# Kernel optimization log

Hardware: AMD Instinct MI355X
Metric: run time of the kernel (lower is better)

## Reference

```python
import jax, jax.numpy as jnp
import numpy as np

D_MODEL = 1024
N_HEAD = 16
HEAD_DIM = D_MODEL // N_HEAD


def setup_inputs() -> dict:
    key = jax.random.key(0)
    k1, k2, k3 = jax.random.split(key, 3)
    B, T = 2, 2048
    x = jax.random.normal(k1, (B, T, D_MODEL), dtype=jnp.float32)
    # nn.MultiheadAttention packed in-projection: (3*D, D), xavier-like scale
    w_in = jax.random.normal(k2, (3 * D_MODEL, D_MODEL), dtype=jnp.float32) * (1.0 / np.sqrt(D_MODEL))
    b_in = jnp.zeros((3 * D_MODEL,), dtype=jnp.float32)
    w_out = jax.random.normal(k3, (D_MODEL, D_MODEL), dtype=jnp.float32) * (1.0 / np.sqrt(D_MODEL))
    b_out = jnp.zeros((D_MODEL,), dtype=jnp.float32)
    return {"x": x, "w_in": w_in, "b_in": b_in, "w_out": w_out, "b_out": b_out}


def reference(x, w_in, b_in, w_out, b_out):
    B, T, D = x.shape
    H, hd = N_HEAD, HEAD_DIM
    # packed QKV projection (torch Linear convention: y = x @ W.T + b)
    qkv = x @ w_in.T + b_in                      # [B, T, 3D]
    q, k, v = jnp.split(qkv, 3, axis=-1)
    # [B, H, T, hd]
    q = q.reshape(B, T, H, hd).transpose(0, 2, 1, 3)
    k = k.reshape(B, T, H, hd).transpose(0, 2, 1, 3)
    v = v.reshape(B, T, H, hd).transpose(0, 2, 1, 3)
    scale = 1.0 / np.sqrt(hd).astype(np.float32)
    scores = jnp.einsum("bhqd,bhkd->bhqk", q * scale, k)  # [B, H, T, T]
    causal = jnp.tril(jnp.ones((T, T), dtype=bool))
    scores = jnp.where(causal, scores, jnp.finfo(scores.dtype).min)
    attn = jax.nn.softmax(scores, axis=-1)
    ctx = jnp.einsum("bhqk,bhkd->bhqd", attn, v)           # [B, H, T, hd]
    ctx = ctx.transpose(0, 2, 1, 3).reshape(B, T, D)
    return ctx @ w_out.T + b_out
```

## Files before the change

kernel.cpp:

```cpp
#include <hip/hip_runtime.h>


#define T_SEQ 2048
#define D_MODEL 1024
#define NEG_BIG (-1.0e30f)
#define Q_SCALE 0.18033688f

typedef float f32x4 __attribute__((ext_vector_type(4)));
typedef short s16x8 __attribute__((ext_vector_type(8)));
typedef __bf16 bf16x8 __attribute__((ext_vector_type(8)));

__device__ __forceinline__ f32x4 mfma16(s16x8 a, s16x8 b, f32x4 c) {
    return __builtin_amdgcn_mfma_f32_16x16x32_bf16(
        __builtin_bit_cast(bf16x8, a), __builtin_bit_cast(bf16x8, b), c, 0, 0, 0);
}

__device__ __forceinline__ short f2bf(float f) {
    unsigned int u = __float_as_uint(f);
    u += 0x7fffu + ((u >> 16) & 1u);
    return (short)(u >> 16);
}
__device__ __forceinline__ unsigned f2bfu(float f) {
    unsigned int u = __float_as_uint(f);
    u += 0x7fffu + ((u >> 16) & 1u);
    return u >> 16;
}
__device__ __forceinline__ unsigned f2bfu_fast(float f) {
    return (__float_as_uint(f) + 0x8000u) >> 16;
}
__device__ __forceinline__ float bf2f(short s) {
    return __uint_as_float(((unsigned int)(unsigned short)s) << 16);
}

__device__ __forceinline__ void async_lds16(const short* g, short* l) {
    __builtin_amdgcn_global_load_lds(
        (const __attribute__((address_space(1))) unsigned int*)g,
        (__attribute__((address_space(3))) unsigned int*)l, 16, 0, 0);
}

#define N_X   4194304
#define N_WI  3145728
#define N_BI  3072
#define N_WO  1048576
#define N_BO  1024
#define V_X   (N_X  / 4)
#define V_WI  (N_WI / 4)
#define V_BI  (N_BI / 4)
#define V_WO  (N_WO / 4)
#define V_BO  (N_BO / 4)
#define V_TOT (V_X + V_WI + V_BI + V_WO + V_BO)

__global__ __launch_bounds__(256) void canon_all_kernel(
    const float* __restrict__ x, const float* __restrict__ wi,
    const float* __restrict__ bi, const float* __restrict__ wo,
    const float* __restrict__ bo,
    short* __restrict__ xb, short* __restrict__ wib, short* __restrict__ bib,
    short* __restrict__ wob, short* __restrict__ bob)
{
    int i = blockIdx.x * 256 + threadIdx.x;
    if (i >= V_TOT) return;
    const float* src; short* dst; int off;
    if      (i < V_X)                    { src = x;  dst = xb;  off = i; }
    else if (i < V_X+V_WI)               { src = wi; dst = wib; off = i - V_X; }
    else if (i < V_X+V_WI+V_BI)          { src = bi; dst = bib; off = i - V_X - V_WI; }
    else if (i < V_X+V_WI+V_BI+V_WO)     { src = wo; dst = wob; off = i - V_X - V_WI - V_BI; }
    else                                 { src = bo; dst = bob; off = i - V_X - V_WI - V_BI - V_WO; }
    float4 v = ((const float4*)src)[off];
    short4 o = { f2bf(v.x), f2bf(v.y), f2bf(v.z), f2bf(v.w) };
    ((short4*)dst)[off] = o;
}

__global__ __launch_bounds__(256) void gemm_qkv_kernel(
    const short* __restrict__ A, const short* __restrict__ B,
    const short* __restrict__ bias,
    short* __restrict__ qo, short* __restrict__ ko, short* __restrict__ vo)
{
    const int K = 1024;
    alignas(16) __shared__ short As[128][32];
    alignas(16) __shared__ short Bs[128][32];
    const int m0 = blockIdx.x * 128;
    const int n0 = blockIdx.y * 128;
    const int tid = threadIdx.x;
    const int lane = tid & 63;
    const int w = tid >> 6;
    const int wm = (w >> 1) * 64, wn = (w & 1) * 64;
    const int quad = lane >> 4, l16 = lane & 15;

    f32x4 acc[4][4];
    const f32x4 zero = {0.f, 0.f, 0.f, 0.f};
#pragma unroll
    for (int i = 0; i < 4; ++i)
#pragma unroll
        for (int j = 0; j < 4; ++j) acc[i][j] = zero;

    const int lrow = lane >> 2;
    const int lcol = (lane & 3) * 8;
    const short* gA0 = &A[(m0 + w*32      + lrow) * K + lcol];
    const short* gA1 = &A[(m0 + w*32 + 16 + lrow) * K + lcol];
    const short* gB0 = &B[(n0 + w*32      + lrow) * K + lcol];
    const short* gB1 = &B[(n0 + w*32 + 16 + lrow) * K + lcol];
    short* lA0 = &As[w*32][0];
    short* lA1 = &As[w*32 + 16][0];
    short* lB0 = &Bs[w*32][0];
    short* lB1 = &Bs[w*32 + 16][0];

    for (int k0 = 0; k0 < K; k0 += 32) {
        __syncthreads();
        async_lds16(gA0 + k0, lA0);
        async_lds16(gA1 + k0, lA1);
        async_lds16(gB0 + k0, lB0);
        async_lds16(gB1 + k0, lB1);
        __syncthreads();

        s16x8 af[4], bfr[4];
#pragma unroll
        for (int i = 0; i < 4; ++i) af[i]  = *(const s16x8*)&As[wm + i*16 + l16][quad*8];
#pragma unroll
        for (int j = 0; j < 4; ++j) bfr[j] = *(const s16x8*)&Bs[wn + j*16 + l16][quad*8];
#pragma unroll
        for (int i = 0; i < 4; ++i)
#pragma unroll
            for (int j = 0; j < 4; ++j)
                acc[i][j] = mfma16(af[i], bfr[j], acc[i][j]);
    }

#pragma unroll
    for (int j = 0; j < 4; ++j) {
        int n = n0 + wn + j*16 + l16;
        float bi = bf2f(bias[n]);
        int which = n >> 10;
        short* dst = (which == 0) ? qo : (which == 1) ? ko : vo;
        float scl = (which == 0) ? Q_SCALE : 1.0f;
        int h = (n >> 6) & 15, d = n & 63;
#pragma unroll
        for (int i = 0; i < 4; ++i) {
#pragma unroll
            for (int r = 0; r < 4; ++r) {
                int m = m0 + wm + i*16 + quad*4 + r;
                int b = m >> 11, t = m & 2047;
                float v = (acc[i][j][r] + bi) * scl;
                dst[(((b*16 + h) * 2048) + t) * 64 + d] = f2bf(v);
            }
        }
    }
}

__global__ __launch_bounds__(256) void transpose_v_kernel(
    const short* __restrict__ V, short* __restrict__ Vt)
{
    alignas(16) __shared__ short buf[64][72];
    const int bh = blockIdx.x;
    const int t0 = blockIdx.y * 64;
    const int tid = threadIdx.x;
    const int r = tid >> 2;
    const int c = (tid & 3) * 16;

    const short* src = V + ((size_t)bh * T_SEQ + t0) * 64;
    *(float4*)&buf[r][c]     = *(const float4*)&src[r * 64 + c];
    *(float4*)&buf[r][c + 8] = *(const float4*)&src[r * 64 + c + 8];
    __syncthreads();

    s16x8 o0, o1;
#pragma unroll
    for (int k2 = 0; k2 < 8; ++k2) {
        o0[k2] = buf[c + k2][r];
        o1[k2] = buf[c + 8 + k2][r];
    }
    short* dst = Vt + ((size_t)bh * 64 + r) * T_SEQ + t0;
    *(s16x8*)&dst[c]     = o0;
    *(s16x8*)&dst[c + 8] = o1;
}

__global__ __launch_bounds__(256) void attn_kernel(
    const short* __restrict__ Q, const short* __restrict__ K,
    const short* __restrict__ Vt, short* __restrict__ ctx)
{
    alignas(16) __shared__ short Ks[64][72];
    alignas(16) __shared__ short Vs[64][72];
    alignas(16) __shared__ short Pl[4][32][72];

    const int bh = blockIdx.x;
    const int qt = 15 - (int)blockIdx.y;
    const int qbase = qt * 128;
    const int tid = threadIdx.x;
    const int w = tid >> 6, lane = tid & 63;
    const int quad = lane >> 4, l16 = lane & 15;
    const int b = bh >> 4, h = bh & 15;

    const short* Qb  = Q  + bh * T_SEQ * 64;
    const short* Kb  = K  + bh * T_SEQ * 64;
    const short* Vbt = Vt + (size_t)bh * 64 * T_SEQ;

    s16x8 qa0[2], qa1[2];
#pragma unroll
    for (int qs = 0; qs < 2; ++qs) {
        const short* qrow = Qb + (qbase + qs*64 + w*16 + l16) * 64;
        qa0[qs] = *(const s16x8*)(qrow + quad*8);
        qa1[qs] = *(const s16x8*)(qrow + 32 + quad*8);
    }

    const f32x4 zero = {0.f, 0.f, 0.f, 0.f};
    f32x4 o[2][4];
#pragma unroll
    for (int qs = 0; qs < 2; ++qs)
#pragma unroll
        for (int dt = 0; dt < 4; ++dt) o[qs][dt] = zero;
    float lsum[2] = {0.f, 0.f};

    const int sr = tid >> 2;
    const int sc = (tid & 3) * 16;

    for (int s0 = 0; s0 <= qbase + 64; s0 += 64) {
        __syncthreads();
        *(float4*)&Ks[sr][sc]     = *(const float4*)&Kb[(s0 + sr) * 64 + sc];
        *(float4*)&Ks[sr][sc + 8] = *(const float4*)&Kb[(s0 + sr) * 64 + sc + 8];
        *(float4*)&Vs[sr][sc]     = *(const float4*)&Vbt[(size_t)sr * T_SEQ + s0 + sc];
        *(float4*)&Vs[sr][sc + 8] = *(const float4*)&Vbt[(size_t)sr * T_SEQ + s0 + sc + 8];
        __syncthreads();

        const bool f0 = (s0 <= qbase);

        s16x8 ka0[4], ka1[4];
#pragma unroll
        for (int sub = 0; sub < 4; ++sub) {
            ka0[sub] = *(const s16x8*)&Ks[sub*16 + l16][quad*8];
            ka1[sub] = *(const s16x8*)&Ks[sub*16 + l16][32 + quad*8];
        }

#pragma unroll
        for (int qs = 0; qs < 2; ++qs) {
            if (qs == 0 && !f0) continue;
            const int fqb = qbase + qs*64;
            const int qg = fqb + w*16 + l16;
#pragma unroll
            for (int sub = 0; sub < 4; ++sub) {
                f32x4 S = mfma16(ka1[sub], qa1[qs], mfma16(ka0[sub], qa0[qs], zero));
                if (s0 == fqb) {
                    int sb = s0 + sub*16 + quad*4;
#pragma unroll
                    for (int r = 0; r < 4; ++r)
                        if (sb + r > qg) S[r] = NEG_BIG;
                }
                float p0 = exp2f(S[0]), p1 = exp2f(S[1]);
                float p2 = exp2f(S[2]), p3 = exp2f(S[3]);
                lsum[qs] += (p0 + p1) + (p2 + p3);
                uint2 pk;
                pk.x = f2bfu_fast(p0) | (f2bfu_fast(p1) << 16);
                pk.y = f2bfu_fast(p2) | (f2bfu_fast(p3) << 16);
                *(uint2*)&Pl[w][qs*16 + l16][sub*16 + quad*4] = pk;
            }
        }

        s16x8 va0[4], va1[4];
#pragma unroll
        for (int dt = 0; dt < 4; ++dt) {
            va0[dt] = *(const s16x8*)&Vs[dt*16 + l16][quad*8];
            va1[dt] = *(const s16x8*)&Vs[dt*16 + l16][32 + quad*8];
        }

#pragma unroll
        for (int qs = 0; qs < 2; ++qs) {
            if (qs == 0 && !f0) continue;
            s16x8 pb0 = *(const s16x8*)&Pl[w][qs*16 + l16][quad*8];
            s16x8 pb1 = *(const s16x8*)&Pl[w][qs*16 + l16][32 + quad*8];
#pragma unroll
            for (int dt = 0; dt < 4; ++dt)
                o[qs][dt] = mfma16(va1[dt], pb1, mfma16(va0[dt], pb0, o[qs][dt]));
        }
    }

#pragma unroll
    for (int qs = 0; qs < 2; ++qs) {
        float l = lsum[qs];
        l += __shfl_xor(l, 16, 64);
        l += __shfl_xor(l, 32, 64);
        float inv = 1.0f / l;
        int qg = qbase + qs*64 + w*16 + l16;
        int base = (b * T_SEQ + qg) * D_MODEL + h * 64;
#pragma unroll
        for (int dt = 0; dt < 4; ++dt) {
            uint2 pk;
            pk.x = f2bfu(o[qs][dt][0] * inv) | (f2bfu(o[qs][dt][1] * inv) << 16);
            pk.y = f2bfu(o[qs][dt][2] * inv) | (f2bfu(o[qs][dt][3] * inv) << 16);
            *(uint2*)&ctx[base + dt*16 + quad*4] = pk;
        }
    }
}

__global__ __launch_bounds__(256) void gemm_out_kernel(
    const short* __restrict__ A, const short* __restrict__ B,
    const short* __restrict__ bias, float* __restrict__ out)
{
    const int K = 1024;
    alignas(16) __shared__ short As[128][32];
    alignas(16) __shared__ short Bs[64][32];
    const int m0 = blockIdx.x * 128;
    const int n0 = blockIdx.y * 64;
    const int tid = threadIdx.x;
    const int lane = tid & 63;
    const int w = tid >> 6;
    const int wm = (w >> 1) * 64, wn = (w & 1) * 32;
    const int quad = lane >> 4, l16 = lane & 15;

    f32x4 acc[4][2];
    const f32x4 zero = {0.f, 0.f, 0.f, 0.f};
#pragma unroll
    for (int i = 0; i < 4; ++i)
#pragma unroll
        for (int j = 0; j < 2; ++j) acc[i][j] = zero;

    const int lrow = lane >> 2;
    const int lcol = (lane & 3) * 8;
    const short* gA0 = &A[(m0 + w*32      + lrow) * K + lcol];
    const short* gA1 = &A[(m0 + w*32 + 16 + lrow) * K + lcol];
    const short* gB0 = &B[(n0 + w*16      + lrow) * K + lcol];
    short* lA0 = &As[w*32][0];
    short* lA1 = &As[w*32 + 16][0];
    short* lB0 = &Bs[w*16][0];

    for (int k0 = 0; k0 < K; k0 += 32) {
        __syncthreads();
        async_lds16(gA0 + k0, lA0);
        async_lds16(gA1 + k0, lA1);
        async_lds16(gB0 + k0, lB0);
        __syncthreads();

        s16x8 af[4], bfr[2];
#pragma unroll
        for (int i = 0; i < 4; ++i) af[i]  = *(const s16x8*)&As[wm + i*16 + l16][quad*8];
#pragma unroll
        for (int j = 0; j < 2; ++j) bfr[j] = *(const s16x8*)&Bs[wn + j*16 + l16][quad*8];
#pragma unroll
        for (int i = 0; i < 4; ++i)
#pragma unroll
            for (int j = 0; j < 2; ++j)
                acc[i][j] = mfma16(af[i], bfr[j], acc[i][j]);
    }

#pragma unroll
    for (int j = 0; j < 2; ++j) {
        int n = n0 + wn + j*16 + l16;
        float bi = bf2f(bias[n]);
#pragma unroll
        for (int i = 0; i < 4; ++i) {
#pragma unroll
            for (int r = 0; r < 4; ++r) {
                int m = m0 + wm + i*16 + quad*4 + r;
                out[m * 1024 + n] = acc[i][j][r] + bi;
            }
        }
    }
}

extern "C" void kernel_launch(void* const* d_in, const int* in_sizes, int n_in,
                              void* d_out, int out_size, void* d_ws, size_t ws_size,
                              hipStream_t stream) {
    float* out = (float*)d_out;
    char* ws = (char*)d_ws;

    const size_t MB = 1u << 20;
    short* xb     = (short*)(ws);
    short* w_inb  = (short*)(ws + 8*MB);
    short* b_inb  = (short*)(ws + 14*MB);
    short* w_outb = (short*)(ws + 15*MB);
    short* b_outb = (short*)(ws + 17*MB);
    short* qb     = (short*)(ws + 18*MB);
    short* kb     = (short*)(ws + 26*MB);
    short* vb     = (short*)(ws + 34*MB);
    short* ctxb   = (short*)(ws + 42*MB);
    short* vtb    = xb;

    canon_all_kernel<<<(V_TOT + 255) / 256, 256, 0, stream>>>(
        (const float*)d_in[0], (const float*)d_in[1], (const float*)d_in[2],
        (const float*)d_in[3], (const float*)d_in[4],
        xb, w_inb, b_inb, w_outb, b_outb);

    gemm_qkv_kernel<<<dim3(32, 24), 256, 0, stream>>>(xb, w_inb, b_inb, qb, kb, vb);
    transpose_v_kernel<<<dim3(32, 32), 256, 0, stream>>>(vb, vtb);
    attn_kernel<<<dim3(32, 16), 256, 0, stream>>>(qb, kb, vtb, ctxb);
    gemm_out_kernel<<<dim3(32, 16), 256, 0, stream>>>(ctxb, w_outb, b_outb, out);
}
```

Measured before the change: 199.3 us.

## Split attention into single-wave blocks loading K/V directly from global

The attention kernel goes from 256-thread blocks covering 128 query rows to 64-thread single-wave blocks covering 32 query rows, launched as 2048 blocks ordered heaviest first. K and V fragments are now read straight from global memory into registers instead of being staged through shared memory, which removes the __syncthreads barriers and the LDS copy. In exchange, K/V reuse across waves now depends on cache hits rather than shared memory, so global/L2 traffic for K and V rises.

```diff
diff --git a/kernel.cpp b/kernel.cpp
--- a/kernel.cpp
+++ b/kernel.cpp
@@ -171,19 +171,17 @@
     *(s16x8*)&dst[c + 8] = o1;
 }
 
-__global__ __launch_bounds__(256) void attn_kernel(
+__global__ __launch_bounds__(64, 4) void attn_kernel(
     const short* __restrict__ Q, const short* __restrict__ K,
     const short* __restrict__ Vt, short* __restrict__ ctx)
 {
-    alignas(16) __shared__ short Ks[64][72];
-    alignas(16) __shared__ short Vs[64][72];
-    alignas(16) __shared__ short Pl[4][32][72];
-
-    const int bh = blockIdx.x;
-    const int qt = 15 - (int)blockIdx.y;
-    const int qbase = qt * 128;
-    const int tid = threadIdx.x;
-    const int w = tid >> 6, lane = tid & 63;
+    alignas(16) __shared__ short Pl[32][72];
+
+    const int bid = blockIdx.x;
+    const int bh = bid & 31;
+    const int qf = 63 - (bid >> 5);
+    const int qr0 = qf * 32;
+    const int lane = threadIdx.x;
     const int quad = lane >> 4, l16 = lane & 15;
     const int b = bh >> 4, h = bh & 15;
 
@@ -194,7 +192,7 @@
     s16x8 qa0[2], qa1[2];
 #pragma unroll
     for (int qs = 0; qs < 2; ++qs) {
-        const short* qrow = Qb + (qbase + qs*64 + w*16 + l16) * 64;
+        const short* qrow = Qb + (qr0 + qs*16 + l16) * 64;
         qa0[qs] = *(const s16x8*)(qrow + quad*8);
         qa1[qs] = *(const s16x8*)(qrow + 32 + quad*8);
     }
@@ -207,35 +205,24 @@
         for (int dt = 0; dt < 4; ++dt) o[qs][dt] = zero;
     float lsum[2] = {0.f, 0.f};
 
-    const int sr = tid >> 2;
-    const int sc = (tid & 3) * 16;
-
-    for (int s0 = 0; s0 <= qbase + 64; s0 += 64) {
-        __syncthreads();
-        *(float4*)&Ks[sr][sc]     = *(const float4*)&Kb[(s0 + sr) * 64 + sc];
-        *(float4*)&Ks[sr][sc + 8] = *(const float4*)&Kb[(s0 + sr) * 64 + sc + 8];
-        *(float4*)&Vs[sr][sc]     = *(const float4*)&Vbt[(size_t)sr * T_SEQ + s0 + sc];
-        *(float4*)&Vs[sr][sc + 8] = *(const float4*)&Vbt[(size_t)sr * T_SEQ + s0 + sc + 8];
-        __syncthreads();
-
-        const bool f0 = (s0 <= qbase);
-
+    const int s_max = (qr0 >> 6) << 6;
+
+    for (int s0 = 0; s0 <= s_max; s0 += 64) {
         s16x8 ka0[4], ka1[4];
 #pragma unroll
         for (int sub = 0; sub < 4; ++sub) {
-            ka0[sub] = *(const s16x8*)&Ks[sub*16 + l16][quad*8];
-            ka1[sub] = *(const s16x8*)&Ks[sub*16 + l16][32 + quad*8];
+            const short* kr = &Kb[(s0 + sub*16 + l16) * 64 + quad*8];
+            ka0[sub] = *(const s16x8*)kr;
+            ka1[sub] = *(const s16x8*)(kr + 32);
         }
 
 #pragma unroll
         for (int qs = 0; qs < 2; ++qs) {
-            if (qs == 0 && !f0) continue;
-            const int fqb = qbase + qs*64;
-            const int qg = fqb + w*16 + l16;
+            const int qg = qr0 + qs*16 + l16;
 #pragma unroll
             for (int sub = 0; sub < 4; ++sub) {
                 f32x4 S = mfma16(ka1[sub], qa1[qs], mfma16(ka0[sub], qa0[qs], zero));
-                if (s0 == fqb) {
+                if (s0 == s_max) {
                     int sb = s0 + sub*16 + quad*4;
 #pragma unroll
                     for (int r = 0; r < 4; ++r)
@@ -247,22 +234,22 @@
                 uint2 pk;
                 pk.x = f2bfu_fast(p0) | (f2bfu_fast(p1) << 16);
                 pk.y = f2bfu_fast(p2) | (f2bfu_fast(p3) << 16);
-                *(uint2*)&Pl[w][qs*16 + l16][sub*16 + quad*4] = pk;
+                *(uint2*)&Pl[qs*16 + l16][sub*16 + quad*4] = pk;
             }
         }
 
         s16x8 va0[4], va1[4];
 #pragma unroll
         for (int dt = 0; dt < 4; ++dt) {
-            va0[dt] = *(const s16x8*)&Vs[dt*16 + l16][quad*8];
-            va1[dt] = *(const s16x8*)&Vs[dt*16 + l16][32 + quad*8];
+            const short* vr = &Vbt[(size_t)(dt*16 + l16) * T_SEQ + s0 + quad*8];
+            va0[dt] = *(const s16x8*)vr;
+            va1[dt] = *(const s16x8*)(vr + 32);
         }
 
 #pragma unroll
         for (int qs = 0; qs < 2; ++qs) {
-            if (qs == 0 && !f0) continue;
-            s16x8 pb0 = *(const s16x8*)&Pl[w][qs*16 + l16][quad*8];
-            s16x8 pb1 = *(const s16x8*)&Pl[w][qs*16 + l16][32 + quad*8];
+            s16x8 pb0 = *(const s16x8*)&Pl[qs*16 + l16][quad*8];
+            s16x8 pb1 = *(const s16x8*)&Pl[qs*16 + l16][32 + quad*8];
 #pragma unroll
             for (int dt = 0; dt < 4; ++dt)
                 o[qs][dt] = mfma16(va1[dt], pb1, mfma16(va0[dt], pb0, o[qs][dt]));
@@ -275,7 +262,7 @@
         l += __shfl_xor(l, 16, 64);
         l += __shfl_xor(l, 32, 64);
         float inv = 1.0f / l;
-        int qg = qbase + qs*64 + w*16 + l16;
+        int qg = qr0 + qs*16 + l16;
         int base = (b * T_SEQ + qg) * D_MODEL + h * 64;
 #pragma unroll
         for (int dt = 0; dt < 4; ++dt) {
@@ -313,7 +300,7 @@
     const int lcol = (lane & 3) * 8;
     const short* gA0 = &A[(m0 + w*32      + lrow) * K + lcol];
     const short* gA1 = &A[(m0 + w*32 + 16 + lrow) * K + lcol];
-    const short* gB0 = &B[(n0 + w*16      + lrow) * K + lcol];
+    const short* gB0 = &B[(n0 + w*16 + lrow) * K + lcol];
     short* lA0 = &As[w*32][0];
     short* lA1 = &As[w*32 + 16][0];
     short* lB0 = &Bs[w*16][0];
@@ -377,6 +364,6 @@
 
     gemm_qkv_kernel<<<dim3(32, 24), 256, 0, stream>>>(xb, w_inb, b_inb, qb, kb, vb);
     transpose_v_kernel<<<dim3(32, 32), 256, 0, stream>>>(vb, vtb);
-    attn_kernel<<<dim3(32, 16), 256, 0, stream>>>(qb, kb, vtb, ctxb);
+    attn_kernel<<<2048, 64, 0, stream>>>(qb, kb, vtb, ctxb);
     gemm_out_kernel<<<dim3(32, 16), 256, 0, stream>>>(ctxb, w_outb, b_outb, out);
 }
```

Result: slower. 213.3 us (+7.0%).
